# Optimization experiments

Measured on AMD Instinct MI355X. Metric: run time of the kernel, lower is better.

## Reference

```python
import jax, jax.numpy as jnp
import numpy as np

H = 4          # hidden_size
NUM_LAYERS = 5
SEQ = 610
BATCH = 128


def _lstm_layer(x, w_i, w_h, bi, bh):
    # x: [B, T, I]; w_i: [4H, I]; w_h: [4H, H]; bi, bh: [4H]
    # PyTorch gate order: i, f, g, o
    B = x.shape[0]
    b = bi + bh

    def step(carry, xt):
        h, c = carry
        gates = xt @ w_i.T + h @ w_h.T + b          # [B, 4H]
        i, f, g, o = jnp.split(gates, 4, axis=-1)
        c = jax.nn.sigmoid(f) * c + jax.nn.sigmoid(i) * jnp.tanh(g)
        h = jax.nn.sigmoid(o) * jnp.tanh(c)
        return (h, c), h

    h0 = jnp.zeros((B, H), x.dtype)
    c0 = jnp.zeros((B, H), x.dtype)
    (_, _), hs = jax.lax.scan(step, (h0, c0), jnp.swapaxes(x, 0, 1))  # hs: [T, B, H]
    return jnp.swapaxes(hs, 0, 1)                   # [B, T, H]


def setup_inputs() -> dict:
    key = jax.random.key(0)
    ks = jax.random.split(key, 10)
    s = 1.0 / np.sqrt(H)  # PyTorch default uniform(-1/sqrt(H), 1/sqrt(H))
    u = lambda k, shape: jax.random.uniform(k, shape, jnp.float32, -s, s)
    return {
        "x": jax.random.normal(ks[0], (BATCH, SEQ, 2), jnp.float32),
        "w_ih0": u(ks[1], (4 * H, 2)),
        "w_ih": u(ks[2], (NUM_LAYERS - 1, 4 * H, H)),
        "w_hh": u(ks[3], (NUM_LAYERS, 4 * H, H)),
        "b_ih": u(ks[4], (NUM_LAYERS, 4 * H)),
        "b_hh": u(ks[5], (NUM_LAYERS, 4 * H)),
        "w_lin": u(ks[6], (1, H)),
        "b_lin": u(ks[7], (1,)),
        "w_fc": jax.random.uniform(ks[8], (5, SEQ), jnp.float32, -1.0 / np.sqrt(SEQ), 1.0 / np.sqrt(SEQ)),
        "b_fc": jax.random.uniform(ks[9], (5,), jnp.float32, -1.0 / np.sqrt(SEQ), 1.0 / np.sqrt(SEQ)),
    }


def reference(x, w_ih0, w_ih, w_hh, b_ih, b_hh, w_lin, b_lin, w_fc, b_fc):
    # 5-layer stacked LSTM, zero initial state (as on the module's first call)
    out = _lstm_layer(x, w_ih0, w_hh[0], b_ih[0], b_hh[0])
    for l in range(NUM_LAYERS - 1):
        out = _lstm_layer(out, w_ih[l], w_hh[l + 1], b_ih[l + 1], b_hh[l + 1])
    # per-timestep Linear(4 -> 1) then cat along dim 1 -> [B, T]
    t = (out @ w_lin.T + b_lin)[..., 0]             # [B, 610]
    return t @ w_fc.T + b_fc                         # [B, 5]
```

## Files before the change

kernel.cpp:

```cpp
#include <hip/hip_runtime.h>
#include <math.h>

#define H 4
#define NL 5
#define SEQ 610
#define BATCH 128
#define TICKS (SEQ + NL - 1)

template<int CTRL, bool BC>
__device__ __forceinline__ float dpp(float old_, float src) {
    return __int_as_float(__builtin_amdgcn_update_dpp(
        __float_as_int(old_), __float_as_int(src), CTRL, 0xF, 0xF, BC));
}

__global__ __launch_bounds__(64) void lstm_cyc_kernel(
    const float* __restrict__ x,
    const float* __restrict__ w_ih0,
    const float* __restrict__ w_ih,
    const float* __restrict__ w_hh,
    const float* __restrict__ b_ih,
    const float* __restrict__ b_hh,
    const float* __restrict__ w_lin,
    const float* __restrict__ b_lin,
    const float* __restrict__ w_fc,
    const float* __restrict__ b_fc,
    float* __restrict__ out)
{
    __shared__ float lds_x[2 * SEQ * 2 + 16];
    __shared__ float lds_wfc[5 * SEQ + 16];

    const int lane = threadIdx.x;
    const int half = lane >> 5;
    const int r    = lane & 31;
    const int l    = r >> 2;
    const int k    = r & 3;
    const int lw   = l > 4 ? 4 : l;
    const bool is_l0 = (l == 0);
    const int  b   = blockIdx.x * 2 + half;

    #pragma unroll
    for (int hh = 0; hh < 2; ++hh) {
        const float4* src = (const float4*)(x + (size_t)(blockIdx.x * 2 + hh) * (SEQ * 2));
        float4* dst = (float4*)&lds_x[hh * (SEQ * 2)];
        for (int i = lane; i < (SEQ * 2) / 4; i += 64) dst[i] = src[i];
    }
    {
        const float2* src = (const float2*)w_fc;
        float2* dst = (float2*)lds_wfc;
        for (int i = lane; i < (5 * SEQ) / 2; i += 64) dst[i] = src[i];
    }
    __syncthreads();

    float wi[4][4], wh[4][4], bias[4];
    #pragma unroll
    for (int j = 0; j < 4; ++j) {
        const float s = (j == 2) ? 2.8853900817779268f
                                 : -1.4426950408889634f;
        const int row = j * H + k;
        if (lw == 0) {
            wi[j][0] = w_ih0[row * 2 + 0] * s;
            wi[j][1] = w_ih0[row * 2 + 1] * s;
            wi[j][2] = 0.f; wi[j][3] = 0.f;
        } else {
            const float4 v = *(const float4*)&w_ih[((lw - 1) * 16 + row) * 4];
            wi[j][0] = v.x * s; wi[j][1] = v.y * s; wi[j][2] = v.z * s; wi[j][3] = v.w * s;
        }
        const float4 u = *(const float4*)&w_hh[(lw * 16 + row) * 4];
        wh[j][0] = u.x * s; wh[j][1] = u.y * s; wh[j][2] = u.z * s; wh[j][3] = u.w * s;
        bias[j] = (b_ih[lw * 16 + row] + b_hh[lw * 16 + row]) * s;
    }
    const float wl0 = w_lin[0], wl1 = w_lin[1], wl2 = w_lin[2], wl3 = w_lin[3];
    const float bl  = b_lin[0];

    const int xbase = half * (SEQ * 2);
    const int wfcA_base = k * SEQ;

    float c = 0.f;
    float q0 = 0.f, q1 = 0.f, q2 = 0.f, q3 = 0.f;
    float wfcA = 0.f, wfcB = 0.f, accA = 0.f, accB = 0.f;
    float pre0, pre1, pre2, pre3;
    {
        const float2 xv0 = *(const float2*)&lds_x[xbase];
        const float xq0 = is_l0 ? xv0.x : 0.f;
        const float xq1 = is_l0 ? xv0.y : 0.f;
        pre0 = fmaf(wi[0][1], xq1, fmaf(wi[0][0], xq0, bias[0]));
        pre1 = fmaf(wi[1][1], xq1, fmaf(wi[1][0], xq0, bias[1]));
        pre2 = fmaf(wi[2][1], xq1, fmaf(wi[2][0], xq0, bias[2]));
        pre3 = fmaf(wi[3][1], xq1, fmaf(wi[3][0], xq0, bias[3]));
    }

    #define TICK_BODY(GATED)                                                          \
    {                                                                                 \
                                           \
        int tn = tau + 1;                                                             \
        int t4 = tau - 3;                                                             \
        if (GATED) t4 = t4 < 0 ? 0 : t4;                                              \
        const float2 nx = *(const float2*)&lds_x[xbase + tn * 2];                     \
        const float nwA = lds_wfc[wfcA_base + t4];                                    \
        const float nwB = lds_wfc[4 * SEQ + t4];                                      \
                                              \
        const float g0 = fmaf(wh[0][3], q3, fmaf(wh[0][2], q2, fmaf(wh[0][1], q1, fmaf(wh[0][0], q0, pre0)))); \
        const float g1 = fmaf(wh[1][3], q3, fmaf(wh[1][2], q2, fmaf(wh[1][1], q1, fmaf(wh[1][0], q0, pre1)))); \
        const float g2 = fmaf(wh[2][3], q3, fmaf(wh[2][2], q2, fmaf(wh[2][1], q1, fmaf(wh[2][0], q0, pre2)))); \
        const float g3 = fmaf(wh[3][3], q3, fmaf(wh[3][2], q2, fmaf(wh[3][1], q1, fmaf(wh[3][0], q0, pre3)))); \
        const float Ai = 1.f + __builtin_amdgcn_exp2f(g0);                            \
        const float Af = 1.f + __builtin_amdgcn_exp2f(g1);                            \
        const float Dg = 1.f + __builtin_amdgcn_exp2f(g2);                            \
        const float Ao = 1.f + __builtin_amdgcn_exp2f(g3);                            \
        const float M   = Ai * Dg;                                                    \
        const float den = M * Af;                                                     \
        const float num = fmaf(c, M, Af * (Dg - 2.f));                                \
        float cn = num * __builtin_amdgcn_rcpf(den);                                  \
        unsigned tt = (unsigned)(tau - l);                                            \
        if (GATED) cn = (tt < SEQ) ? cn : 0.f;                                        \
        c = cn;                                                                       \
        const float Dc = 1.f + __builtin_amdgcn_exp2f(c * 2.8853900817779268f);       \
        const float h  = (Dc - 2.f) * __builtin_amdgcn_rcpf(Ao * Dc);                 \
                                                          \
        const float nq0 = dpp<0x00, true>(0.f, h);                                    \
        const float nq1 = dpp<0x55, true>(0.f, h);                                    \
        const float nq2 = dpp<0xAA, true>(0.f, h);                                    \
        const float nq3 = dpp<0xFF, true>(0.f, h);                                    \
                                \
        float p0 = dpp<0x142, true>(0.f, nq0); p0 = dpp<0x114, false>(p0, nq0);       \
        float p1 = dpp<0x142, true>(0.f, nq1); p1 = dpp<0x114, false>(p1, nq1);       \
        float p2 = dpp<0x142, true>(0.f, nq2); p2 = dpp<0x114, false>(p2, nq2);       \
        float p3 = dpp<0x142, true>(0.f, nq3); p3 = dpp<0x114, false>(p3, nq3);       \
        const float xq0 = is_l0 ? nx.x : p0;                                          \
        const float xq1 = is_l0 ? nx.y : p1;                                          \
                        \
        pre0 = fmaf(wi[0][3], p3, fmaf(wi[0][2], p2, fmaf(wi[0][1], xq1, fmaf(wi[0][0], xq0, bias[0])))); \
        pre1 = fmaf(wi[1][3], p3, fmaf(wi[1][2], p2, fmaf(wi[1][1], xq1, fmaf(wi[1][0], xq0, bias[1])))); \
        pre2 = fmaf(wi[2][3], p3, fmaf(wi[2][2], p2, fmaf(wi[2][1], xq1, fmaf(wi[2][0], xq0, bias[2])))); \
        pre3 = fmaf(wi[3][3], p3, fmaf(wi[3][2], p2, fmaf(wi[3][1], xq1, fmaf(wi[3][0], xq0, bias[3])))); \
                                    \
        float tval = fmaf(nq3, wl3, bl);                                              \
        tval = fmaf(nq2, wl2, tval);                                                  \
        tval = fmaf(nq1, wl1, tval);                                                  \
        tval = fmaf(nq0, wl0, tval);                                                  \
        if (GATED) tval = (tt < SEQ) ? tval : 0.f;                                    \
        accA = fmaf(tval, wfcA, accA);                                                \
        accB = fmaf(tval, wfcB, accB);                                                \
        q0 = nq0; q1 = nq1; q2 = nq2; q3 = nq3;                                       \
        wfcA = nwA; wfcB = nwB;                                                       \
    }

    for (int tau = 0; tau < 4; ++tau) TICK_BODY(true);
    #pragma unroll 2
    for (int tau = 4; tau < TICKS; ++tau) TICK_BODY(false);
    #undef TICK_BODY

    if (r >= 16 && r < 20) {
        out[b * 5 + k] = accA + b_fc[k];
        if (k == 0) out[b * 5 + 4] = accB + b_fc[4];
    }
}

extern "C" void kernel_launch(void* const* d_in, const int* in_sizes, int n_in,
                              void* d_out, int out_size, void* d_ws, size_t ws_size,
                              hipStream_t stream)
{
    const float* x     = (const float*)d_in[0];
    const float* w_ih0 = (const float*)d_in[1];
    const float* w_ih  = (const float*)d_in[2];
    const float* w_hh  = (const float*)d_in[3];
    const float* b_ih  = (const float*)d_in[4];
    const float* b_hh  = (const float*)d_in[5];
    const float* w_lin = (const float*)d_in[6];
    const float* b_lin = (const float*)d_in[7];
    const float* w_fc  = (const float*)d_in[8];
    const float* b_fc  = (const float*)d_in[9];
    float* out = (float*)d_out;

    lstm_cyc_kernel<<<dim3(BATCH / 2), dim3(64), 0, stream>>>(
        x, w_ih0, w_ih, w_hh, b_ih, b_hh, w_lin, b_lin, w_fc, b_fc, out);
}
```

Before: 170.2 us.

## Skew layer wavefront by two ticks to take cross-layer shuffle off the critical path

The layer pipeline changes from a one-tick skew to a two-tick skew (layer l processes timestep tau-2l). The next layer's input projection now uses the previous tick's hidden state, so the row_shr DPP shuffles run in parallel with the recurrent path instead of after it. The w_fc weights are also stored interleaved so each tick needs one float2 LDS load instead of two scalar loads. In exchange the loop runs 619 ticks instead of 614, and the prologue and head-gating logic are more involved.

```diff
diff --git a/kernel.cpp b/kernel.cpp
--- a/kernel.cpp
+++ b/kernel.cpp
@@ -5,15 +5,16 @@
 #define NL 5
 #define SEQ 610
 #define BATCH 128
-#define TICKS (SEQ + NL - 1)
+#define NITER 619
+#define HEAD 10
 
 template<int CTRL, bool BC>
-__device__ __forceinline__ float dpp(float old_, float src) {
+__device__ __forceinline__ float dpp1(float old_, float src) {
     return __int_as_float(__builtin_amdgcn_update_dpp(
         __float_as_int(old_), __float_as_int(src), CTRL, 0xF, 0xF, BC));
 }
 
-__global__ __launch_bounds__(64) void lstm_cyc_kernel(
+__global__ __launch_bounds__(64) void lstm_sp_kernel(
     const float* __restrict__ x,
     const float* __restrict__ w_ih0,
     const float* __restrict__ w_ih,
@@ -26,8 +27,8 @@
     const float* __restrict__ b_fc,
     float* __restrict__ out)
 {
-    __shared__ float lds_x[2 * SEQ * 2 + 16];
-    __shared__ float lds_wfc[5 * SEQ + 16];
+    __shared__ float lds_x[2 * SEQ * 2 + 24];
+    __shared__ float lds_wfcp[4 * SEQ * 2];
 
     const int lane = threadIdx.x;
     const int half = lane >> 5;
@@ -36,7 +37,7 @@
     const int k    = r & 3;
     const int lw   = l > 4 ? 4 : l;
     const bool is_l0 = (l == 0);
-    const int  b   = blockIdx.x * 2 + half;
+    const int row  = blockIdx.x * 2 + half;
 
     #pragma unroll
     for (int hh = 0; hh < 2; ++hh) {
@@ -44,10 +45,12 @@
         float4* dst = (float4*)&lds_x[hh * (SEQ * 2)];
         for (int i = lane; i < (SEQ * 2) / 4; i += 64) dst[i] = src[i];
     }
-    {
-        const float2* src = (const float2*)w_fc;
-        float2* dst = (float2*)lds_wfc;
-        for (int i = lane; i < (5 * SEQ) / 2; i += 64) dst[i] = src[i];
+    #pragma unroll
+    for (int kk = 0; kk < 4; ++kk) {
+        for (int t = lane; t < SEQ; t += 64) {
+            lds_wfcp[(kk * SEQ + t) * 2 + 0] = w_fc[kk * SEQ + t];
+            lds_wfcp[(kk * SEQ + t) * 2 + 1] = w_fc[4 * SEQ + t];
+        }
     }
     __syncthreads();
 
@@ -56,31 +59,31 @@
     for (int j = 0; j < 4; ++j) {
         const float s = (j == 2) ? 2.8853900817779268f
                                  : -1.4426950408889634f;
-        const int row = j * H + k;
+        const int wrow = j * H + k;
         if (lw == 0) {
-            wi[j][0] = w_ih0[row * 2 + 0] * s;
-            wi[j][1] = w_ih0[row * 2 + 1] * s;
+            wi[j][0] = w_ih0[wrow * 2 + 0] * s;
+            wi[j][1] = w_ih0[wrow * 2 + 1] * s;
             wi[j][2] = 0.f; wi[j][3] = 0.f;
         } else {
-            const float4 v = *(const float4*)&w_ih[((lw - 1) * 16 + row) * 4];
+            const float4 v = *(const float4*)&w_ih[((lw - 1) * 16 + wrow) * 4];
             wi[j][0] = v.x * s; wi[j][1] = v.y * s; wi[j][2] = v.z * s; wi[j][3] = v.w * s;
         }
-        const float4 u = *(const float4*)&w_hh[(lw * 16 + row) * 4];
+        const float4 u = *(const float4*)&w_hh[(lw * 16 + wrow) * 4];
         wh[j][0] = u.x * s; wh[j][1] = u.y * s; wh[j][2] = u.z * s; wh[j][3] = u.w * s;
-        bias[j] = (b_ih[lw * 16 + row] + b_hh[lw * 16 + row]) * s;
+        bias[j] = (b_ih[lw * 16 + wrow] + b_hh[lw * 16 + wrow]) * s;
     }
     const float wl0 = w_lin[0], wl1 = w_lin[1], wl2 = w_lin[2], wl3 = w_lin[3];
     const float bl  = b_lin[0];
 
-    const int xbase = half * (SEQ * 2);
-    const int wfcA_base = k * SEQ;
+    const int xb     = half * (SEQ * 2);
+    const int wpbase = k * SEQ;
 
     float c = 0.f;
     float q0 = 0.f, q1 = 0.f, q2 = 0.f, q3 = 0.f;
-    float wfcA = 0.f, wfcB = 0.f, accA = 0.f, accB = 0.f;
+    float accA = 0.f, accB = 0.f;
     float pre0, pre1, pre2, pre3;
     {
-        const float2 xv0 = *(const float2*)&lds_x[xbase];
+        const float2 xv0 = *(const float2*)&lds_x[xb];
         const float xq0 = is_l0 ? xv0.x : 0.f;
         const float xq1 = is_l0 ? xv0.y : 0.f;
         pre0 = fmaf(wi[0][1], xq1, fmaf(wi[0][0], xq0, bias[0]));
@@ -89,20 +92,20 @@
         pre3 = fmaf(wi[3][1], xq1, fmaf(wi[3][0], xq0, bias[3]));
     }
 
-    #define TICK_BODY(GATED)                                                          \
+    #define TICK_BODY(tau_, GATED)                                                    \
     {                                                                                 \
-                                           \
-        int tn = tau + 1;                                                             \
-        int t4 = tau - 3;                                                             \
+                                   \
+        const float2 nx = *(const float2*)&lds_x[xb + ((tau_) + 1) * 2];              \
+        int t4 = (tau_) - 9;                                                          \
         if (GATED) t4 = t4 < 0 ? 0 : t4;                                              \
-        const float2 nx = *(const float2*)&lds_x[xbase + tn * 2];                     \
-        const float nwA = lds_wfc[wfcA_base + t4];                                    \
-        const float nwB = lds_wfc[4 * SEQ + t4];                                      \
+        const float2 wv = *(const float2*)&lds_wfcp[(wpbase + t4) * 2];               \
                                               \
-        const float g0 = fmaf(wh[0][3], q3, fmaf(wh[0][2], q2, fmaf(wh[0][1], q1, fmaf(wh[0][0], q0, pre0)))); \
-        const float g1 = fmaf(wh[1][3], q3, fmaf(wh[1][2], q2, fmaf(wh[1][1], q1, fmaf(wh[1][0], q0, pre1)))); \
-        const float g2 = fmaf(wh[2][3], q3, fmaf(wh[2][2], q2, fmaf(wh[2][1], q1, fmaf(wh[2][0], q0, pre2)))); \
-        const float g3 = fmaf(wh[3][3], q3, fmaf(wh[3][2], q2, fmaf(wh[3][1], q1, fmaf(wh[3][0], q0, pre3)))); \
+        const float oq0 = q0, oq1 = q1, oq2 = q2, oq3 = q3;                           \
+                  \
+        const float g0 = fmaf(wh[0][3], oq3, fmaf(wh[0][2], oq2, fmaf(wh[0][1], oq1, fmaf(wh[0][0], oq0, pre0)))); \
+        const float g1 = fmaf(wh[1][3], oq3, fmaf(wh[1][2], oq2, fmaf(wh[1][1], oq1, fmaf(wh[1][0], oq0, pre1)))); \
+        const float g2 = fmaf(wh[2][3], oq3, fmaf(wh[2][2], oq2, fmaf(wh[2][1], oq1, fmaf(wh[2][0], oq0, pre2)))); \
+        const float g3 = fmaf(wh[3][3], oq3, fmaf(wh[3][2], oq2, fmaf(wh[3][1], oq1, fmaf(wh[3][0], oq0, pre3)))); \
         const float Ai = 1.f + __builtin_amdgcn_exp2f(g0);                            \
         const float Af = 1.f + __builtin_amdgcn_exp2f(g1);                            \
         const float Dg = 1.f + __builtin_amdgcn_exp2f(g2);                            \
@@ -111,48 +114,40 @@
         const float den = M * Af;                                                     \
         const float num = fmaf(c, M, Af * (Dg - 2.f));                                \
         float cn = num * __builtin_amdgcn_rcpf(den);                                  \
-        unsigned tt = (unsigned)(tau - l);                                            \
-        if (GATED) cn = (tt < SEQ) ? cn : 0.f;                                        \
+        if (GATED) { const unsigned tt = (unsigned)((tau_) - 2 * l);                  \
+                     cn = (tt < SEQ) ? cn : 0.f; }                                    \
         c = cn;                                                                       \
         const float Dc = 1.f + __builtin_amdgcn_exp2f(c * 2.8853900817779268f);       \
         const float h  = (Dc - 2.f) * __builtin_amdgcn_rcpf(Ao * Dc);                 \
-                                                          \
-        const float nq0 = dpp<0x00, true>(0.f, h);                                    \
-        const float nq1 = dpp<0x55, true>(0.f, h);                                    \
-        const float nq2 = dpp<0xAA, true>(0.f, h);                                    \
-        const float nq3 = dpp<0xFF, true>(0.f, h);                                    \
-                                \
-        float p0 = dpp<0x142, true>(0.f, nq0); p0 = dpp<0x114, false>(p0, nq0);       \
-        float p1 = dpp<0x142, true>(0.f, nq1); p1 = dpp<0x114, false>(p1, nq1);       \
-        float p2 = dpp<0x142, true>(0.f, nq2); p2 = dpp<0x114, false>(p2, nq2);       \
-        float p3 = dpp<0x142, true>(0.f, nq3); p3 = dpp<0x114, false>(p3, nq3);       \
+        q0 = dpp1<0x00, true>(0.f, h);                                                \
+        q1 = dpp1<0x55, true>(0.f, h);                                                \
+        q2 = dpp1<0xAA, true>(0.f, h);                                                \
+        q3 = dpp1<0xFF, true>(0.f, h);                                                \
+                \
+        float p0 = dpp1<0x142, true>(0.f, oq0); p0 = dpp1<0x114, false>(p0, oq0);     \
+        float p1 = dpp1<0x142, true>(0.f, oq1); p1 = dpp1<0x114, false>(p1, oq1);     \
+        float p2 = dpp1<0x142, true>(0.f, oq2); p2 = dpp1<0x114, false>(p2, oq2);     \
+        float p3 = dpp1<0x142, true>(0.f, oq3); p3 = dpp1<0x114, false>(p3, oq3);     \
         const float xq0 = is_l0 ? nx.x : p0;                                          \
         const float xq1 = is_l0 ? nx.y : p1;                                          \
-                        \
         pre0 = fmaf(wi[0][3], p3, fmaf(wi[0][2], p2, fmaf(wi[0][1], xq1, fmaf(wi[0][0], xq0, bias[0])))); \
         pre1 = fmaf(wi[1][3], p3, fmaf(wi[1][2], p2, fmaf(wi[1][1], xq1, fmaf(wi[1][0], xq0, bias[1])))); \
         pre2 = fmaf(wi[2][3], p3, fmaf(wi[2][2], p2, fmaf(wi[2][1], xq1, fmaf(wi[2][0], xq0, bias[2])))); \
         pre3 = fmaf(wi[3][3], p3, fmaf(wi[3][2], p2, fmaf(wi[3][1], xq1, fmaf(wi[3][0], xq0, bias[3])))); \
-                                    \
-        float tval = fmaf(nq3, wl3, bl);                                              \
-        tval = fmaf(nq2, wl2, tval);                                                  \
-        tval = fmaf(nq1, wl1, tval);                                                  \
-        tval = fmaf(nq0, wl0, tval);                                                  \
-        if (GATED) tval = (tt < SEQ) ? tval : 0.f;                                    \
-        accA = fmaf(tval, wfcA, accA);                                                \
-        accB = fmaf(tval, wfcB, accB);                                                \
-        q0 = nq0; q1 = nq1; q2 = nq2; q3 = nq3;                                       \
-        wfcA = nwA; wfcB = nwB;                                                       \
+        float tval = fmaf(oq0, wl0, fmaf(oq1, wl1, fmaf(oq2, wl2, fmaf(oq3, wl3, bl)))); \
+        if (GATED) tval = ((unsigned)((tau_) - 9) < SEQ) ? tval : 0.f;                \
+        accA = fmaf(tval, wv.x, accA);                                                \
+        accB = fmaf(tval, wv.y, accB);                                                \
     }
 
-    for (int tau = 0; tau < 4; ++tau) TICK_BODY(true);
+    for (int tau = 0; tau < HEAD; ++tau) TICK_BODY(tau, true);
     #pragma unroll 2
-    for (int tau = 4; tau < TICKS; ++tau) TICK_BODY(false);
+    for (int tau = HEAD; tau < NITER; ++tau) TICK_BODY(tau, false);
     #undef TICK_BODY
 
     if (r >= 16 && r < 20) {
-        out[b * 5 + k] = accA + b_fc[k];
-        if (k == 0) out[b * 5 + 4] = accB + b_fc[4];
+        out[row * 5 + k] = accA + b_fc[k];
+        if (k == 0) out[row * 5 + 4] = accB + b_fc[4];
     }
 }
 
@@ -172,6 +167,6 @@
     const float* b_fc  = (const float*)d_in[9];
     float* out = (float*)d_out;
 
-    lstm_cyc_kernel<<<dim3(BATCH / 2), dim3(64), 0, stream>>>(
+    lstm_sp_kernel<<<dim3(BATCH / 2), dim3(64), 0, stream>>>(
         x, w_ih0, w_ih, w_hh, b_ih, b_hh, w_lin, b_lin, w_fc, b_fc, out);
 }
```

Result: slower. 176.6 us (+3.7%).
